# Performance work log

Hardware: AMD Instinct MI355X
Metric: run time of the kernel (lower is better)

Reference implementation:

```python
import jax, jax.numpy as jnp
import numpy as np

SCALE = 5.656854249492381  # sqrt(head_dim=32)


def setup_inputs() -> dict:
    key = jax.random.key(0)
    kq, kk, kv = jax.random.split(key, 3)
    shape = (16, 16, 256, 32)  # [batch, heads, seq, head_dim]
    q = jax.random.normal(kq, shape, dtype=jnp.float16)
    k = jax.random.normal(kk, shape, dtype=jnp.float16)
    v = jax.random.normal(kv, shape, dtype=jnp.float16)
    return {"q": q, "k": k, "v": v}


def reference(q, k, v):
    # scores = q @ k^T / sqrt(d): [b, h, s, s], fp16 matmul then fp32 softmax
    scores = jnp.einsum("bhqd,bhkd->bhqk", q, k) / jnp.float16(SCALE)
    probs = jax.nn.softmax(scores.astype(jnp.float32), axis=-1).astype(jnp.float16)
    out = jnp.einsum("bhqk,bhkd->bhqd", probs, v)  # [b, h, s, d]
    return (out,)
```

## Files before the change

kernel.cpp:

```cpp
#include <hip/hip_runtime.h>


typedef _Float16 f16;
typedef f16 f16x8 __attribute__((ext_vector_type(8)));
typedef float f32x4 __attribute__((ext_vector_type(4)));

#define SEQ 256
#define HD 32
#define SP (SEQ + 8)

__global__ __launch_bounds__(256, 1)
void attn_kernel(const float* __restrict__ Q, const float* __restrict__ K,
                 const float* __restrict__ V, float* __restrict__ O)
{
    __shared__ __align__(16) f16 Vt[HD][SP];
    __shared__ __align__(16) f16 Pb[4][16][SP];

    const int tid  = threadIdx.x;
    const int wave = tid >> 6;
    const int lane = tid & 63;
    const int l15  = lane & 15;
    const int quad = lane >> 4;

    const size_t base = (size_t)blockIdx.x * (SEQ * HD);
    const float* q = Q + base;
    const float* k = K + base;
    const float* v = V + base;
    float*       o = O + base;

    #pragma unroll
    for (int it = 0; it < 8; ++it) {
        int vec = tid + it * 256;
        int r = vec >> 3;
        int c = (vec & 7) * 4;
        f32x4 val = *(const f32x4*)(v + r * HD + c);
        #pragma unroll
        for (int j = 0; j < 4; ++j)
            Vt[c + j][r] = (f16)val[j];
    }
    __syncthreads();

    f16x8 vb[8][2];
    #pragma unroll
    for (int c = 0; c < 8; ++c)
        #pragma unroll
        for (int h = 0; h < 2; ++h)
            vb[c][h] = *(const f16x8*)(&Vt[h * 16 + l15][c * 32 + quad * 8]);

    f16x8 kf[16];
    #pragma unroll
    for (int t = 0; t < 16; ++t) {
        const float* kp = k + (t * 16 + l15) * HD + quad * 8;
        f32x4 a = *(const f32x4*)(kp);
        f32x4 b = *(const f32x4*)(kp + 4);
        #pragma unroll
        for (int j = 0; j < 4; ++j) { kf[t][j] = (f16)a[j]; kf[t][4 + j] = (f16)b[j]; }
    }

    const float inv_scale = 1.0f / 5.65625f;

    #pragma unroll 1
    for (int qi = 0; qi < 4; ++qi) {
        const int qt = wave * 4 + qi;
        const float* qp = q + (qt * 16 + l15) * HD + quad * 8;
        f32x4 a = *(const f32x4*)(qp);
        f32x4 b = *(const f32x4*)(qp + 4);
        f16x8 qa;
        #pragma unroll
        for (int j = 0; j < 4; ++j) { qa[j] = (f16)a[j]; qa[4 + j] = (f16)b[j]; }

        f32x4 sc[16];
        #pragma unroll
        for (int t = 0; t < 16; ++t) {
            f32x4 z = {0.f, 0.f, 0.f, 0.f};
            sc[t] = __builtin_amdgcn_mfma_f32_16x16x32_f16(qa, kf[t], z, 0, 0, 0);
        }

        #pragma unroll
        for (int r4 = 0; r4 < 4; ++r4) {
            float sv[16];
            float m = -1e30f;
            #pragma unroll
            for (int t = 0; t < 16; ++t) {
                sv[t] = sc[t][r4] * inv_scale;
                m = fmaxf(m, sv[t]);
            }
            #pragma unroll
            for (int off = 1; off < 16; off <<= 1)
                m = fmaxf(m, __shfl_xor(m, off));
            float sum = 0.f;
            #pragma unroll
            for (int t = 0; t < 16; ++t) {
                sv[t] = __expf(sv[t] - m);
                sum += sv[t];
            }
            #pragma unroll
            for (int off = 1; off < 16; off <<= 1)
                sum += __shfl_xor(sum, off);
            const float rs = 1.0f / sum;
            const int row = quad * 4 + r4;
            #pragma unroll
            for (int t = 0; t < 16; ++t)
                Pb[wave][row][t * 16 + l15] = (f16)(sv[t] * rs);
        }
        __syncthreads();

        f32x4 oacc0 = {0.f, 0.f, 0.f, 0.f};
        f32x4 oacc1 = {0.f, 0.f, 0.f, 0.f};
        #pragma unroll
        for (int c = 0; c < 8; ++c) {
            f16x8 pa = *(const f16x8*)(&Pb[wave][l15][c * 32 + quad * 8]);
            oacc0 = __builtin_amdgcn_mfma_f32_16x16x32_f16(pa, vb[c][0], oacc0, 0, 0, 0);
            oacc1 = __builtin_amdgcn_mfma_f32_16x16x32_f16(pa, vb[c][1], oacc1, 0, 0, 0);
        }
        __syncthreads();

        #pragma unroll
        for (int r4 = 0; r4 < 4; ++r4) {
            const int row = qt * 16 + quad * 4 + r4;
            o[row * HD + l15]      = (float)(f16)oacc0[r4];
            o[row * HD + 16 + l15] = (float)(f16)oacc1[r4];
        }
    }
}

extern "C" void kernel_launch(void* const* d_in, const int* in_sizes, int n_in,
                              void* d_out, int out_size, void* d_ws, size_t ws_size,
                              hipStream_t stream) {
    const float* q = (const float*)d_in[0];
    const float* k = (const float*)d_in[1];
    const float* v = (const float*)d_in[2];
    float* o = (float*)d_out;
    const int bh = in_sizes[0] / (SEQ * HD);
    attn_kernel<<<bh, 256, 0, stream>>>(q, k, v, o);
}
```

Measured before the change: 91.59 us.

## Split each head across two blocks, stage K in LDS, defer softmax normalization

Launches two blocks per batch-head, each handling half the query tiles, so the grid doubles and occupancy rises (launch bounds allow two blocks per CU). K is converted once to fp16 into shared memory and read per tile, replacing the large per-thread register array. Softmax normalization moves to the output, and the per-wave __syncthreads barriers are removed since each wave uses its own P buffer. The price is that K and V are loaded and converted twice per head, and normalizing after PV changes rounding slightly versus the reference. The grid decode hardcodes 256 slices.

After: 80.84 us. 11.7% less time.

```diff
diff --git a/kernel.cpp b/kernel.cpp
--- a/kernel.cpp
+++ b/kernel.cpp
@@ -2,17 +2,23 @@
 
 
 typedef _Float16 f16;
+typedef f16 f16x4 __attribute__((ext_vector_type(4)));
 typedef f16 f16x8 __attribute__((ext_vector_type(8)));
 typedef float f32x4 __attribute__((ext_vector_type(4)));
+typedef f16x8 f16x8_u __attribute__((may_alias));
+typedef f16x4 f16x4_u __attribute__((may_alias));
+typedef f32x4 f32x4_u __attribute__((may_alias));
 
 #define SEQ 256
 #define HD 32
-#define SP (SEQ + 8)
+#define KP 40
+#define SP 264
 
-__global__ __launch_bounds__(256, 1)
+__global__ __launch_bounds__(256, 2)
 void attn_kernel(const float* __restrict__ Q, const float* __restrict__ K,
                  const float* __restrict__ V, float* __restrict__ O)
 {
+    __shared__ __align__(16) f16 Ks[SEQ][KP];
     __shared__ __align__(16) f16 Vt[HD][SP];
     __shared__ __align__(16) f16 Pb[4][16][SP];
 
@@ -22,7 +28,10 @@
     const int l15  = lane & 15;
     const int quad = lane >> 4;
 
-    const size_t base = (size_t)blockIdx.x * (SEQ * HD);
+    const int slice = blockIdx.x & 255;
+    const int half  = blockIdx.x >> 8;
+
+    const size_t base = (size_t)slice * (SEQ * HD);
     const float* q = Q + base;
     const float* k = K + base;
     const float* v = V + base;
@@ -32,11 +41,15 @@
     for (int it = 0; it < 8; ++it) {
         int vec = tid + it * 256;
         int r = vec >> 3;
-        int c = (vec & 7) * 4;
-        f32x4 val = *(const f32x4*)(v + r * HD + c);
+        int c = (vec & 7) << 2;
+        f32x4 kv = *(const f32x4_u*)(k + r * HD + c);
+        f32x4 vv = *(const f32x4_u*)(v + r * HD + c);
+        f16x4 kh;
         #pragma unroll
-        for (int j = 0; j < 4; ++j)
-            Vt[c + j][r] = (f16)val[j];
+        for (int j = 0; j < 4; ++j) kh[j] = (f16)kv[j];
+        *(f16x4_u*)(&Ks[r][c]) = kh;
+        #pragma unroll
+        for (int j = 0; j < 4; ++j) Vt[c + j][r] = (f16)vv[j];
     }
     __syncthreads();
 
@@ -45,26 +58,16 @@
     for (int c = 0; c < 8; ++c)
         #pragma unroll
         for (int h = 0; h < 2; ++h)
-            vb[c][h] = *(const f16x8*)(&Vt[h * 16 + l15][c * 32 + quad * 8]);
-
-    f16x8 kf[16];
-    #pragma unroll
-    for (int t = 0; t < 16; ++t) {
-        const float* kp = k + (t * 16 + l15) * HD + quad * 8;
-        f32x4 a = *(const f32x4*)(kp);
-        f32x4 b = *(const f32x4*)(kp + 4);
-        #pragma unroll
-        for (int j = 0; j < 4; ++j) { kf[t][j] = (f16)a[j]; kf[t][4 + j] = (f16)b[j]; }
-    }
+            vb[c][h] = *(const f16x8_u*)(&Vt[h * 16 + l15][c * 32 + quad * 8]);
 
     const float inv_scale = 1.0f / 5.65625f;
 
     #pragma unroll 1
-    for (int qi = 0; qi < 4; ++qi) {
-        const int qt = wave * 4 + qi;
+    for (int qi = 0; qi < 2; ++qi) {
+        const int qt = half * 8 + wave * 2 + qi;
         const float* qp = q + (qt * 16 + l15) * HD + quad * 8;
-        f32x4 a = *(const f32x4*)(qp);
-        f32x4 b = *(const f32x4*)(qp + 4);
+        f32x4 a = *(const f32x4_u*)(qp);
+        f32x4 b = *(const f32x4_u*)(qp + 4);
         f16x8 qa;
         #pragma unroll
         for (int j = 0; j < 4; ++j) { qa[j] = (f16)a[j]; qa[4 + j] = (f16)b[j]; }
@@ -72,10 +75,12 @@
         f32x4 sc[16];
         #pragma unroll
         for (int t = 0; t < 16; ++t) {
+            f16x8 kf = *(const f16x8_u*)(&Ks[t * 16 + l15][quad * 8]);
             f32x4 z = {0.f, 0.f, 0.f, 0.f};
-            sc[t] = __builtin_amdgcn_mfma_f32_16x16x32_f16(qa, kf[t], z, 0, 0, 0);
+            sc[t] = __builtin_amdgcn_mfma_f32_16x16x32_f16(qa, kf, z, 0, 0, 0);
         }
 
+        float rs4[4];
         #pragma unroll
         for (int r4 = 0; r4 < 4; ++r4) {
             float sv[16];
@@ -97,29 +102,27 @@
             #pragma unroll
             for (int off = 1; off < 16; off <<= 1)
                 sum += __shfl_xor(sum, off);
-            const float rs = 1.0f / sum;
+            rs4[r4] = 1.0f / sum;
             const int row = quad * 4 + r4;
             #pragma unroll
             for (int t = 0; t < 16; ++t)
-                Pb[wave][row][t * 16 + l15] = (f16)(sv[t] * rs);
+                Pb[wave][row][t * 16 + l15] = (f16)sv[t];
         }
-        __syncthreads();
 
-        f32x4 oacc0 = {0.f, 0.f, 0.f, 0.f};
-        f32x4 oacc1 = {0.f, 0.f, 0.f, 0.f};
+        f32x4 o0 = {0.f, 0.f, 0.f, 0.f};
+        f32x4 o1 = {0.f, 0.f, 0.f, 0.f};
         #pragma unroll
         for (int c = 0; c < 8; ++c) {
-            f16x8 pa = *(const f16x8*)(&Pb[wave][l15][c * 32 + quad * 8]);
-            oacc0 = __builtin_amdgcn_mfma_f32_16x16x32_f16(pa, vb[c][0], oacc0, 0, 0, 0);
-            oacc1 = __builtin_amdgcn_mfma_f32_16x16x32_f16(pa, vb[c][1], oacc1, 0, 0, 0);
+            f16x8 pa = *(const f16x8_u*)(&Pb[wave][l15][c * 32 + quad * 8]);
+            o0 = __builtin_amdgcn_mfma_f32_16x16x32_f16(pa, vb[c][0], o0, 0, 0, 0);
+            o1 = __builtin_amdgcn_mfma_f32_16x16x32_f16(pa, vb[c][1], o1, 0, 0, 0);
         }
-        __syncthreads();
 
         #pragma unroll
         for (int r4 = 0; r4 < 4; ++r4) {
             const int row = qt * 16 + quad * 4 + r4;
-            o[row * HD + l15]      = (float)(f16)oacc0[r4];
-            o[row * HD + 16 + l15] = (float)(f16)oacc1[r4];
+            o[row * HD + l15]      = (float)(f16)(o0[r4] * rs4[r4]);
+            o[row * HD + 16 + l15] = (float)(f16)(o1[r4] * rs4[r4]);
         }
     }
 }
@@ -132,5 +135,5 @@
     const float* v = (const float*)d_in[2];
     float* o = (float*)d_out;
     const int bh = in_sizes[0] / (SEQ * HD);
-    attn_kernel<<<bh, 256, 0, stream>>>(q, k, v, o);
+    attn_kernel<<<bh * 2, 256, 0, stream>>>(q, k, v, o);
 }
```
